# Performance work log

Hardware: AMD Instinct MI355X
Metric: run time of the kernel (lower is better)

## Reference

```python
import jax, jax.numpy as jnp
import numpy as np

K_MASK = -2.3819763e+38
NUM_KV_HEADS = 4
SOFT_CAP = 50.0
WINDOW = 1024
ROPE_BASE = 10000.0
ROPE_SCALE = 1.0


def rms_norm(x, scale=None, eps=1e-6):
    var = jnp.mean(jnp.square(x), axis=-1, keepdims=True)
    normed = x * jax.lax.rsqrt(var + eps)
    if scale is not None:
        normed = normed * (1.0 + scale)
    return normed


def apply_rope(x, positions):
    # x: [B, T, N, H], positions: [B, T]
    head_dim = x.shape[-1]
    fraction = 2.0 * jnp.arange(head_dim // 2, dtype=jnp.float32) / head_dim
    timescale = ROPE_BASE ** fraction  # [H/2]
    sinusoid = positions[..., None, None].astype(jnp.float32) / timescale / ROPE_SCALE  # [B,T,1,H/2]
    sin, cos = jnp.sin(sinusoid), jnp.cos(sinusoid)
    first, second = jnp.split(x, 2, axis=-1)
    return jnp.concatenate([first * cos - second * sin,
                            second * cos + first * sin], axis=-1).astype(x.dtype)


def setup_inputs() -> dict:
    key = jax.random.key(0)
    ks = jax.random.split(key, 8)
    B, T, D, N, K, H, F = 2, 2048, 2048, 8, NUM_KV_HEADS, 256, 8192
    CACHE = 4096
    x = jax.random.normal(ks[0], (B, T, D), dtype=jnp.float32)
    segment_pos = jnp.broadcast_to(jnp.arange(T, dtype=jnp.int32)[None, :], (B, T))
    # causal mask over cache slots: after scatter, slot s (< T) holds position s; slots >= T are empty
    s_idx = jnp.arange(CACHE)
    t_idx = jnp.arange(T)
    attn_mask = (s_idx[None, :] <= t_idx[:, None]) & (s_idx[None, :] < T)
    attn_mask = jnp.broadcast_to(attn_mask[None], (B, T, CACHE))
    cache_k = jnp.zeros((B, CACHE, K, H), dtype=jnp.float32)
    cache_v = jnp.zeros((B, CACHE, K, H), dtype=jnp.float32)
    cache_positions = jnp.zeros((B, CACHE), dtype=jnp.int32)
    end_index = jnp.zeros((B,), dtype=jnp.int32)
    w_q = jax.random.normal(ks[1], (N, D, H), dtype=jnp.float32) * 0.02
    w_kv = jax.random.normal(ks[2], (2, K, D, H), dtype=jnp.float32) * 0.02
    w_attn_vec = jax.random.normal(ks[3], (N, H, D), dtype=jnp.float32) * 0.02
    w_gating = jax.random.normal(ks[4], (2, F, D), dtype=jnp.float32) * 0.02
    w_linear = jax.random.normal(ks[5], (F, D), dtype=jnp.float32) * 0.02
    return {
        'x': x, 'segment_pos': segment_pos, 'attn_mask': attn_mask,
        'cache_k': cache_k, 'cache_v': cache_v,
        'cache_positions': cache_positions, 'end_index': end_index,
        'w_q': w_q, 'w_kv': w_kv, 'w_attn_vec': w_attn_vec,
        'q_norm_scale': jnp.zeros((H,), dtype=jnp.float32),
        'k_norm_scale': jnp.zeros((H,), dtype=jnp.float32),
        'pre_attn_scale': jnp.zeros((D,), dtype=jnp.float32),
        'post_attn_scale': jnp.zeros((D,), dtype=jnp.float32),
        'pre_ffw_scale': jnp.zeros((D,), dtype=jnp.float32),
        'post_ffw_scale': jnp.zeros((D,), dtype=jnp.float32),
        'w_gating': w_gating, 'w_linear': w_linear,
        'skip_scale': jnp.ones((1,), dtype=jnp.float32),
    }


def reference(x, segment_pos, attn_mask, cache_k, cache_v, cache_positions, end_index,
              w_q, w_kv, w_attn_vec, q_norm_scale, k_norm_scale,
              pre_attn_scale, post_attn_scale, pre_ffw_scale, post_ffw_scale,
              w_gating, w_linear, skip_scale):
    B, T, D = x.shape
    cache_size = cache_v.shape[1]

    h = rms_norm(x, pre_attn_scale)

    # --- attention ---
    q = jnp.einsum('BTD,NDH->BTNH', h, w_q)
    q = rms_norm(q, q_norm_scale)
    q = apply_rope(q, segment_pos)

    k, v = jnp.einsum('BSD,CKDH->CBSKH', h, w_kv)
    k = rms_norm(k, k_norm_scale)
    v = rms_norm(v, None)
    k = apply_rope(k, segment_pos)

    # KV-cache scatter (ring-buffer indexing)
    idx = (end_index[:, None] + jnp.arange(T)[None, :]) % cache_size  # [B,T]
    bidx = jnp.arange(B)[:, None]
    v = cache_v.at[bidx, idx].set(v)              # [B,S,K,H]
    k = cache_k.at[bidx, idx].set(k)
    cache_pos = cache_positions.at[bidx, idx].set(segment_pos)  # [B,S]

    # GQA logits
    N, H = q.shape[2], q.shape[3]
    G = N // NUM_KV_HEADS
    qg = q.reshape(B, T, NUM_KV_HEADS, G, H)
    logits = jnp.einsum('BTKGH,BSKH->BTKGS', qg, k).reshape(B, T, N, cache_size)

    # soft cap
    logits = jnp.tanh(logits / SOFT_CAP) * SOFT_CAP

    # sliding-window mask against cache positions
    sliding = (cache_pos[:, None, :] > segment_pos[:, :, None] - WINDOW) & \
              (cache_pos[:, None, :] < segment_pos[:, :, None] + WINDOW)  # [B,T,S]
    mask = attn_mask & sliding

    padded = jnp.where(mask[:, :, None, :], logits, K_MASK)
    probs = jax.nn.softmax(padded, axis=-1).astype(k.dtype)

    pg = probs.reshape(B, T, NUM_KV_HEADS, G, cache_size)
    encoded = jnp.einsum('BTKGS,BSKH->BTKGH', pg, v).reshape(B, T, N, H)
    attn_out = jnp.einsum('BTNH,NHD->BTD', encoded, w_attn_vec)

    # post-attn norm + residual (skip_scale on the skip connection)
    attn_out = rms_norm(attn_out, post_attn_scale)
    attn_out = x * skip_scale + attn_out

    # --- feed-forward ---
    ffw_in = rms_norm(attn_out, pre_ffw_scale)
    gate = jnp.einsum('BTF,CHF->BTCH', ffw_in, w_gating)  # C=2
    act = jax.nn.gelu(gate[..., 0, :]) * gate[..., 1, :]
    ffw_out = jnp.einsum('BTH,HF->BTF', act, w_linear)
    ffw_out = rms_norm(ffw_out, post_ffw_scale)

    return attn_out + ffw_out
```

## Files before the change

kernel.cpp:

```cpp
#include <hip/hip_runtime.h>


typedef _Float16 h8 __attribute__((ext_vector_type(8)));
typedef _Float16 h4 __attribute__((ext_vector_type(4)));
typedef float f4 __attribute__((ext_vector_type(4)));

#define BDIM 2
#define TDIM 2048
#define DDIM 2048
#define NQ 8
#define NKV 4
#define HDIM 256
#define FDIM 8192
#define MROWS (BDIM * TDIM)
#define WINDOW 1024

__device__ inline float gelu_tanh(float x) {
  return 0.5f * x * (1.f + tanhf(0.7978845608028654f * (x + 0.044715f * x * x * x)));
}

__device__ __forceinline__ void g2l16(const _Float16* g, _Float16* l) {
  __builtin_amdgcn_global_load_lds(
      (const __attribute__((address_space(1))) void*)g,
      (__attribute__((address_space(3))) void*)l, 16, 0, 0);
}

__device__ inline float block_sum(float v, float* sbuf) {
#pragma unroll
  for (int off = 32; off; off >>= 1) v += __shfl_xor(v, off, 64);
  __syncthreads();
  if ((threadIdx.x & 63) == 0) sbuf[threadIdx.x >> 6] = v;
  __syncthreads();
  return sbuf[0] + sbuf[1] + sbuf[2] + sbuf[3];
}

template <int EPI>
__global__ __launch_bounds__(256, 2) void gemm_bt(
    const _Float16* __restrict__ A, const _Float16* __restrict__ Bt,
    void* __restrict__ Cout, const _Float16* __restrict__ aux,
    int M, int Nc, int K) {
  __shared__ _Float16 As[128 * 32];
  __shared__ _Float16 Bs[128 * 32];
  const int tid = threadIdx.x;
  const int m0 = blockIdx.y * 128, n0 = blockIdx.x * 128;
  const int w = tid >> 6, lane = tid & 63;
  const int l16 = lane & 15, quad = lane >> 4;
  const int wm = (w >> 1) * 64, wn = (w & 1) * 64;

  f4 acc[4][4];
#pragma unroll
  for (int i = 0; i < 4; i++)
#pragma unroll
    for (int j = 0; j < 4; j++) {
      acc[i][j][0] = 0.f; acc[i][j][1] = 0.f; acc[i][j][2] = 0.f; acc[i][j][3] = 0.f;
    }

  const int lrow = lane >> 2, lcol = (lane & 3) * 8;
  const _Float16* Ag = A + (size_t)(m0 + w * 32 + lrow) * K + lcol;
  const _Float16* Bg = Bt + (size_t)(n0 + w * 32 + lrow) * K + lcol;
  _Float16* AsW = &As[(w * 32) * 32];
  _Float16* BsW = &Bs[(w * 32) * 32];

  for (int k0 = 0; k0 < K; k0 += 32) {
    __syncthreads();
    g2l16(Ag + k0,                AsW);
    g2l16(Ag + (size_t)16 * K + k0, AsW + 16 * 32);
    g2l16(Bg + k0,                BsW);
    g2l16(Bg + (size_t)16 * K + k0, BsW + 16 * 32);
    __syncthreads();
    h8 af[4], bf[4];
#pragma unroll
    for (int i = 0; i < 4; i++) af[i] = *(const h8*)&As[(wm + i * 16 + l16) * 32 + quad * 8];
#pragma unroll
    for (int i = 0; i < 4; i++) bf[i] = *(const h8*)&Bs[(wn + i * 16 + l16) * 32 + quad * 8];
#pragma unroll
    for (int mi = 0; mi < 4; mi++)
#pragma unroll
      for (int ni = 0; ni < 4; ni++)
        acc[mi][ni] = __builtin_amdgcn_mfma_f32_16x16x32_f16(af[mi], bf[ni], acc[mi][ni], 0, 0, 0);
  }

#pragma unroll
  for (int mi = 0; mi < 4; mi++)
#pragma unroll
    for (int ni = 0; ni < 4; ni++)
#pragma unroll
      for (int r = 0; r < 4; r++) {
        const int rg = m0 + wm + mi * 16 + quad * 4 + r;
        const int cg = n0 + wn + ni * 16 + l16;
        const size_t idx = (size_t)rg * Nc + cg;
        float v = acc[mi][ni][r];
        if (EPI == 0) {
          ((float*)Cout)[idx] = v;
        } else if (EPI == 1) {
          ((_Float16*)Cout)[idx] = (_Float16)v;
        } else {
          float g = (float)aux[idx];
          ((_Float16*)Cout)[idx] = (_Float16)(gelu_tanh(g) * v);
        }
      }
}

__global__ __launch_bounds__(256) void transpose_cast_kernel(
    const float* __restrict__ in, _Float16* __restrict__ out,
    int R, int C, size_t in_zstride, size_t out_zstride) {
  __shared__ float tile[64][65];
  const float* ip = in + blockIdx.z * in_zstride;
  _Float16* op = out + blockIdx.z * out_zstride;
  const int cb = blockIdx.x * 64, rb = blockIdx.y * 64;
  const int tx = threadIdx.x & 15, ty = threadIdx.x >> 4;
#pragma unroll
  for (int i = 0; i < 4; i++) {
    f4 v = *(const f4*)&ip[(size_t)(rb + ty + 16 * i) * C + cb + tx * 4];
    tile[ty + 16 * i][tx * 4 + 0] = v[0];
    tile[ty + 16 * i][tx * 4 + 1] = v[1];
    tile[ty + 16 * i][tx * 4 + 2] = v[2];
    tile[ty + 16 * i][tx * 4 + 3] = v[3];
  }
  __syncthreads();
#pragma unroll
  for (int i = 0; i < 4; i++) {
    const int c = ty + 16 * i;
    h4 o;
#pragma unroll
    for (int j = 0; j < 4; j++) o[j] = (_Float16)tile[tx * 4 + j][c];
    *(h4*)&op[(size_t)(cb + c) * R + rb + tx * 4] = o;
  }
}

__global__ void cast_fp16_kernel(const float* __restrict__ in,
                                 _Float16* __restrict__ out, int n4) {
  int i = blockIdx.x * 256 + threadIdx.x;
  if (i < n4) {
    f4 v = ((const f4*)in)[i];
    h4 o;
    o[0] = (_Float16)v[0]; o[1] = (_Float16)v[1];
    o[2] = (_Float16)v[2]; o[3] = (_Float16)v[3];
    ((h4*)out)[i] = o;
  }
}

__global__ __launch_bounds__(256) void rmsnorm_fp16_kernel(
    const float* __restrict__ in, const float* __restrict__ scale,
    _Float16* __restrict__ out) {
  __shared__ float sbuf[4];
  const int row = blockIdx.x, tid = threadIdx.x;
  const float* r = in + (size_t)row * 2048;
  f4 a = ((const f4*)r)[tid];
  f4 b = ((const f4*)r)[tid + 256];
  float ss = a[0]*a[0] + a[1]*a[1] + a[2]*a[2] + a[3]*a[3] +
             b[0]*b[0] + b[1]*b[1] + b[2]*b[2] + b[3]*b[3];
  float tot = block_sum(ss, sbuf);
  float rs = rsqrtf(tot * (1.f / 2048.f) + 1e-6f);
  f4 s0 = ((const f4*)scale)[tid];
  f4 s1 = ((const f4*)scale)[tid + 256];
  h4 o0, o1;
#pragma unroll
  for (int j = 0; j < 4; j++) {
    o0[j] = (_Float16)(a[j] * rs * (1.f + s0[j]));
    o1[j] = (_Float16)(b[j] * rs * (1.f + s1[j]));
  }
  ((h4*)(out + (size_t)row * 2048))[tid] = o0;
  ((h4*)(out + (size_t)row * 2048))[tid + 256] = o1;
}

__global__ __launch_bounds__(256) void headnorm_rope_kernel(
    const float* __restrict__ in, _Float16* __restrict__ out,
    const float* __restrict__ scale, const int* __restrict__ pos_arr,
    int heads, int do_rope, int total) {
  const int inst = blockIdx.x * 4 + (threadIdx.x >> 6);
  if (inst >= total) return;
  const int lane = threadIdx.x & 63;
  const int bt = inst / heads;
  const float* r = in + (size_t)inst * 256;
  f4 v = ((const f4*)r)[lane];
  float ss = v[0]*v[0] + v[1]*v[1] + v[2]*v[2] + v[3]*v[3];
#pragma unroll
  for (int off = 32; off; off >>= 1) ss += __shfl_xor(ss, off, 64);
  const float rs = rsqrtf(ss * (1.f / 256.f) + 1e-6f);
  f4 nv;
  if (scale) {
    f4 sc = ((const f4*)scale)[lane];
#pragma unroll
    for (int j = 0; j < 4; j++) nv[j] = v[j] * rs * (1.f + sc[j]);
  } else {
#pragma unroll
    for (int j = 0; j < 4; j++) nv[j] = v[j] * rs;
  }
  _Float16* o = out + (size_t)inst * 256;
  h4 res;
  if (do_rope) {
    const float pos = (float)pos_arr[bt];
    const bool lo = lane < 32;
#pragma unroll
    for (int j = 0; j < 4; j++) {
      float partner = __shfl_xor(nv[j], 32, 64);
      const int ph = (lane * 4 + j) & 127;
      float it = exp2f((float)ph * -0.103810253f);
      float ang = pos * it;
      float sn, cs;
      sincosf(ang, &sn, &cs);
      float val = lo ? (nv[j] * cs - partner * sn) : (nv[j] * cs + partner * sn);
      res[j] = (_Float16)val;
    }
  } else {
#pragma unroll
    for (int j = 0; j < 4; j++) res[j] = (_Float16)nv[j];
  }
  ((h4*)o)[lane] = res;
}

__global__ __launch_bounds__(256) void transpose_v_kernel(
    const _Float16* __restrict__ vbf, _Float16* __restrict__ vT) {
  __shared__ _Float16 tile[32][33];
  const int z = blockIdx.z;
  const int b = z >> 2, kvh = z & 3;
  const int tb = blockIdx.x * 32, hb = blockIdx.y * 32;
  const int x = threadIdx.x, y = threadIdx.y;
#pragma unroll
  for (int i = 0; i < 4; i++)
    tile[y + 8 * i][x] =
        vbf[(size_t)(b * TDIM + tb + y + 8 * i) * (NKV * HDIM) + kvh * HDIM + hb + x];
  __syncthreads();
#pragma unroll
  for (int i = 0; i < 4; i++)
    vT[((size_t)z * HDIM + hb + y + 8 * i) * TDIM + tb + x] = tile[x][y + 8 * i];
}

__global__ __launch_bounds__(256) void attn_kernel(
    const _Float16* __restrict__ qf, const _Float16* __restrict__ kf,
    const _Float16* __restrict__ vT, _Float16* __restrict__ enc) {
  __shared__ _Float16 Ks[32 * 256];
  __shared__ _Float16 Vs[256 * 32];
  __shared__ _Float16 Ps[4][16 * 32];
  const int t0 = blockIdx.x * 64;
  const int n = blockIdx.y;
  const int b = blockIdx.z;
  const int kvh = n >> 1;
  const int tid = threadIdx.x;
  const int w = tid >> 6, lane = tid & 63, l16 = lane & 15, quad = lane >> 4;

  h8 qfrag[8];
  {
    const int trow = t0 + w * 16 + l16;
    const _Float16* qp =
        qf + ((size_t)(b * TDIM + trow) * (NQ * HDIM)) + n * HDIM + quad * 8;
#pragma unroll
    for (int ks = 0; ks < 8; ks++) qfrag[ks] = *(const h8*)(qp + ks * 32);
  }

  f4 O[16];
#pragma unroll
  for (int i = 0; i < 16; i++) { O[i][0] = 0.f; O[i][1] = 0.f; O[i][2] = 0.f; O[i][3] = 0.f; }
  float m_i[4], l_i[4];
#pragma unroll
  for (int r = 0; r < 4; r++) { m_i[r] = -1e30f; l_i[r] = 0.f; }

  int s_begin = t0 - (WINDOW - 1);
  if (s_begin < 0) s_begin = 0;
  s_begin &= ~31;
  const int s_end = t0 + 64;
  const _Float16* kbase = kf + (size_t)b * TDIM * (NKV * HDIM) + kvh * HDIM;
  const _Float16* vbase = vT + ((size_t)(b * NKV + kvh) * HDIM) * TDIM;

  for (int s0 = s_begin; s0 < s_end; s0 += 32) {
    __syncthreads();
#pragma unroll
    for (int p = 0; p < 4; p++) {
      int g = p * 256 + tid;
      {
        int si = g >> 5, hg = (g & 31) << 3;
        *(h8*)&Ks[si * 256 + hg] = *(const h8*)(kbase + (size_t)(s0 + si) * (NKV * HDIM) + hg);
      }
      {
        int h = g >> 2, sg = (g & 3) << 3;
        *(h8*)&Vs[h * 32 + sg] = *(const h8*)(vbase + (size_t)h * TDIM + s0 + sg);
      }
    }
    __syncthreads();

    float P[2][4], cmax[4];
#pragma unroll
    for (int r = 0; r < 4; r++) cmax[r] = -1e30f;
#pragma unroll
    for (int sc = 0; sc < 2; sc++) {
      f4 lg; lg[0] = 0.f; lg[1] = 0.f; lg[2] = 0.f; lg[3] = 0.f;
#pragma unroll
      for (int ks = 0; ks < 8; ks++) {
        h8 kb = *(const h8*)&Ks[(sc * 16 + l16) * 256 + ks * 32 + quad * 8];
        lg = __builtin_amdgcn_mfma_f32_16x16x32_f16(qfrag[ks], kb, lg, 0, 0, 0);
      }
      const int scol = s0 + sc * 16 + l16;
#pragma unroll
      for (int r = 0; r < 4; r++) {
        const int trow = t0 + w * 16 + quad * 4 + r;
        float xv = 50.f * tanhf(lg[r] * 0.02f);
        bool valid = (scol <= trow) && (scol > trow - WINDOW);
        P[sc][r] = valid ? xv : -1e30f;
        cmax[r] = fmaxf(cmax[r], P[sc][r]);
      }
    }
#pragma unroll
    for (int off = 1; off < 16; off <<= 1)
#pragma unroll
      for (int r = 0; r < 4; r++) cmax[r] = fmaxf(cmax[r], __shfl_xor(cmax[r], off, 16));
    float alpha[4], psum[4];
#pragma unroll
    for (int r = 0; r < 4; r++) {
      float mnew = fmaxf(m_i[r], cmax[r]);
      alpha[r] = __expf(m_i[r] - mnew);
      m_i[r] = mnew;
      psum[r] = 0.f;
    }
#pragma unroll
    for (int sc = 0; sc < 2; sc++)
#pragma unroll
      for (int r = 0; r < 4; r++) {
        float pv = __expf(P[sc][r] - m_i[r]);
        P[sc][r] = pv;
        psum[r] += pv;
      }
#pragma unroll
    for (int off = 1; off < 16; off <<= 1)
#pragma unroll
      for (int r = 0; r < 4; r++) psum[r] += __shfl_xor(psum[r], off, 16);
#pragma unroll
    for (int r = 0; r < 4; r++) l_i[r] = l_i[r] * alpha[r] + psum[r];
#pragma unroll
    for (int i = 0; i < 16; i++)
#pragma unroll
      for (int r = 0; r < 4; r++) O[i][r] *= alpha[r];
#pragma unroll
    for (int sc = 0; sc < 2; sc++)
#pragma unroll
      for (int r = 0; r < 4; r++)
        Ps[w][(quad * 4 + r) * 32 + sc * 16 + l16] = (_Float16)P[sc][r];
    h8 pa = *(const h8*)&Ps[w][l16 * 32 + quad * 8];
#pragma unroll
    for (int ht = 0; ht < 16; ht++) {
      h8 vb = *(const h8*)&Vs[(ht * 16 + l16) * 32 + quad * 8];
      O[ht] = __builtin_amdgcn_mfma_f32_16x16x32_f16(pa, vb, O[ht], 0, 0, 0);
    }
  }

  float invl[4];
#pragma unroll
  for (int r = 0; r < 4; r++) invl[r] = 1.f / l_i[r];
#pragma unroll
  for (int ht = 0; ht < 16; ht++)
#pragma unroll
    for (int r = 0; r < 4; r++) {
      const int trow = t0 + w * 16 + quad * 4 + r;
      enc[((size_t)(b * TDIM + trow)) * (NQ * HDIM) + n * HDIM + ht * 16 + l16] =
          (_Float16)(O[ht][r] * invl[r]);
    }
}

__global__ __launch_bounds__(256) void postattn_kernel(
    const float* __restrict__ attnraw, const float* __restrict__ x,
    const float* __restrict__ post_scale, const float* __restrict__ pre_ffw_scale,
    const float* __restrict__ skip, float* __restrict__ attn_out,
    _Float16* __restrict__ ffw_in) {
  __shared__ float sbuf[4];
  const int row = blockIdx.x, tid = threadIdx.x;
  const float* ar = attnraw + (size_t)row * 2048;
  const float* xr = x + (size_t)row * 2048;
  f4 a0 = ((const f4*)ar)[tid], a1 = ((const f4*)ar)[tid + 256];
  float ss = a0[0]*a0[0] + a0[1]*a0[1] + a0[2]*a0[2] + a0[3]*a0[3] +
             a1[0]*a1[0] + a1[1]*a1[1] + a1[2]*a1[2] + a1[3]*a1[3];
  float tot = block_sum(ss, sbuf);
  float rs = rsqrtf(tot * (1.f / 2048.f) + 1e-6f);
  const float sk = skip[0];
  f4 x0 = ((const f4*)xr)[tid], x1 = ((const f4*)xr)[tid + 256];
  f4 p0 = ((const f4*)post_scale)[tid], p1 = ((const f4*)post_scale)[tid + 256];
  f4 at0, at1;
#pragma unroll
  for (int j = 0; j < 4; j++) {
    at0[j] = x0[j] * sk + a0[j] * rs * (1.f + p0[j]);
    at1[j] = x1[j] * sk + a1[j] * rs * (1.f + p1[j]);
  }
  ((f4*)(attn_out + (size_t)row * 2048))[tid] = at0;
  ((f4*)(attn_out + (size_t)row * 2048))[tid + 256] = at1;
  float ss2 = at0[0]*at0[0] + at0[1]*at0[1] + at0[2]*at0[2] + at0[3]*at0[3] +
              at1[0]*at1[0] + at1[1]*at1[1] + at1[2]*at1[2] + at1[3]*at1[3];
  float tot2 = block_sum(ss2, sbuf);
  float rs2 = rsqrtf(tot2 * (1.f / 2048.f) + 1e-6f);
  f4 f0 = ((const f4*)pre_ffw_scale)[tid], f1 = ((const f4*)pre_ffw_scale)[tid + 256];
  h4 o0, o1;
#pragma unroll
  for (int j = 0; j < 4; j++) {
    o0[j] = (_Float16)(at0[j] * rs2 * (1.f + f0[j]));
    o1[j] = (_Float16)(at1[j] * rs2 * (1.f + f1[j]));
  }
  ((h4*)(ffw_in + (size_t)row * 2048))[tid] = o0;
  ((h4*)(ffw_in + (size_t)row * 2048))[tid + 256] = o1;
}

__global__ __launch_bounds__(256) void final_kernel(
    const float* __restrict__ ffw, const float* __restrict__ attn_out,
    const float* __restrict__ post_ffw_scale, float* __restrict__ out) {
  __shared__ float sbuf[4];
  const int row = blockIdx.x, tid = threadIdx.x;
  const float* fr = ffw + (size_t)row * 2048;
  const float* ar = attn_out + (size_t)row * 2048;
  f4 a0 = ((const f4*)fr)[tid], a1 = ((const f4*)fr)[tid + 256];
  float ss = a0[0]*a0[0] + a0[1]*a0[1] + a0[2]*a0[2] + a0[3]*a0[3] +
             a1[0]*a1[0] + a1[1]*a1[1] + a1[2]*a1[2] + a1[3]*a1[3];
  float tot = block_sum(ss, sbuf);
  float rs = rsqrtf(tot * (1.f / 2048.f) + 1e-6f);
  f4 s0 = ((const f4*)post_ffw_scale)[tid], s1 = ((const f4*)post_ffw_scale)[tid + 256];
  f4 x0 = ((const f4*)ar)[tid], x1 = ((const f4*)ar)[tid + 256];
  f4 o0, o1;
#pragma unroll
  for (int j = 0; j < 4; j++) {
    o0[j] = x0[j] + a0[j] * rs * (1.f + s0[j]);
    o1[j] = x1[j] + a1[j] * rs * (1.f + s1[j]);
  }
  ((f4*)(out + (size_t)row * 2048))[tid] = o0;
  ((f4*)(out + (size_t)row * 2048))[tid + 256] = o1;
}

extern "C" void kernel_launch(void* const* d_in, const int* in_sizes, int n_in,
                              void* d_out, int out_size, void* d_ws, size_t ws_size,
                              hipStream_t stream) {
  (void)in_sizes; (void)n_in; (void)out_size; (void)ws_size;
  const float* x              = (const float*)d_in[0];
  const int*   segment_pos    = (const int*)d_in[1];
  const float* w_q            = (const float*)d_in[7];
  const float* w_kv           = (const float*)d_in[8];
  const float* w_attn_vec     = (const float*)d_in[9];
  const float* q_norm_scale   = (const float*)d_in[10];
  const float* k_norm_scale   = (const float*)d_in[11];
  const float* pre_attn_scale = (const float*)d_in[12];
  const float* post_attn_scale= (const float*)d_in[13];
  const float* pre_ffw_scale  = (const float*)d_in[14];
  const float* post_ffw_scale = (const float*)d_in[15];
  const float* w_gating       = (const float*)d_in[16];
  const float* w_linear       = (const float*)d_in[17];
  const float* skip_scale     = (const float*)d_in[18];

  char* ws = (char*)d_ws;
  const size_t MB = 1024 * 1024;
  _Float16* Wq   = (_Float16*)(ws + 0);
  _Float16* Wk   = (_Float16*)(ws + 8 * MB);
  _Float16* Wv   = (_Float16*)(ws + 12 * MB);
  _Float16* Wo   = (_Float16*)(ws + 0);
  _Float16* Wg   = (_Float16*)(ws + 0);
  _Float16* Wl   = (_Float16*)(ws + 0);
  _Float16* Hbf  = (_Float16*)(ws + 64 * MB);
  float* attnF   = (float*)(ws + 80 * MB);
  float* qf32    = (float*)(ws + 112 * MB);
  float* kf32    = (float*)(ws + 144 * MB);
  float* vf32    = (float*)(ws + 160 * MB);
  _Float16* qbf  = (_Float16*)(ws + 176 * MB);
  _Float16* kbf  = (_Float16*)(ws + 192 * MB);
  _Float16* vbf  = (_Float16*)(ws + 200 * MB);
  _Float16* enc  = (_Float16*)(ws + 208 * MB);
  float* attnraw = (float*)(ws + 224 * MB);
  _Float16* vT   = (_Float16*)(ws + 112 * MB);
  _Float16* gate0= (_Float16*)(ws + 112 * MB);
  _Float16* act  = (_Float16*)(ws + 176 * MB);
  float* ffw     = (float*)(ws + 240 * MB);
  float* outp    = (float*)d_out;

  transpose_cast_kernel<<<dim3(HDIM / 64, DDIM / 64, NQ), 256, 0, stream>>>(
      w_q, Wq, DDIM, HDIM, (size_t)DDIM * HDIM, (size_t)HDIM * DDIM);
  transpose_cast_kernel<<<dim3(HDIM / 64, DDIM / 64, NKV), 256, 0, stream>>>(
      w_kv, Wk, DDIM, HDIM, (size_t)DDIM * HDIM, (size_t)HDIM * DDIM);
  transpose_cast_kernel<<<dim3(HDIM / 64, DDIM / 64, NKV), 256, 0, stream>>>(
      w_kv + (size_t)NKV * DDIM * HDIM, Wv, DDIM, HDIM,
      (size_t)DDIM * HDIM, (size_t)HDIM * DDIM);
  rmsnorm_fp16_kernel<<<MROWS, 256, 0, stream>>>(x, pre_attn_scale, Hbf);
  gemm_bt<0><<<dim3((NQ * HDIM) / 128, MROWS / 128), 256, 0, stream>>>(
      Hbf, Wq, qf32, nullptr, MROWS, NQ * HDIM, DDIM);
  gemm_bt<0><<<dim3((NKV * HDIM) / 128, MROWS / 128), 256, 0, stream>>>(
      Hbf, Wk, kf32, nullptr, MROWS, NKV * HDIM, DDIM);
  gemm_bt<0><<<dim3((NKV * HDIM) / 128, MROWS / 128), 256, 0, stream>>>(
      Hbf, Wv, vf32, nullptr, MROWS, NKV * HDIM, DDIM);
  headnorm_rope_kernel<<<(MROWS * NQ) / 4, 256, 0, stream>>>(
      qf32, qbf, q_norm_scale, segment_pos, NQ, 1, MROWS * NQ);
  headnorm_rope_kernel<<<(MROWS * NKV) / 4, 256, 0, stream>>>(
      kf32, kbf, k_norm_scale, segment_pos, NKV, 1, MROWS * NKV);
  headnorm_rope_kernel<<<(MROWS * NKV) / 4, 256, 0, stream>>>(
      vf32, vbf, nullptr, segment_pos, NKV, 0, MROWS * NKV);
  transpose_v_kernel<<<dim3(TDIM / 32, HDIM / 32, BDIM * NKV), dim3(32, 8), 0, stream>>>(vbf, vT);
  attn_kernel<<<dim3(TDIM / 64, NQ, BDIM), 256, 0, stream>>>(qbf, kbf, vT, enc);
  transpose_cast_kernel<<<dim3(DDIM / 64, (NQ * HDIM) / 64, 1), 256, 0, stream>>>(
      w_attn_vec, Wo, NQ * HDIM, DDIM, 0, 0);
  gemm_bt<0><<<dim3(DDIM / 128, MROWS / 128), 256, 0, stream>>>(
      enc, Wo, attnraw, nullptr, MROWS, DDIM, NQ * HDIM);
  postattn_kernel<<<MROWS, 256, 0, stream>>>(attnraw, x, post_attn_scale,
                                             pre_ffw_scale, skip_scale, attnF, Hbf);
  cast_fp16_kernel<<<(2 * FDIM * DDIM / 4 + 255) / 256, 256, 0, stream>>>(
      w_gating, Wg, 2 * FDIM * DDIM / 4);
  gemm_bt<1><<<dim3(FDIM / 128, MROWS / 128), 256, 0, stream>>>(
      Hbf, Wg, gate0, nullptr, MROWS, FDIM, DDIM);
  gemm_bt<2><<<dim3(FDIM / 128, MROWS / 128), 256, 0, stream>>>(
      Hbf, Wg + (size_t)FDIM * DDIM, act, gate0, MROWS, FDIM, DDIM);
  transpose_cast_kernel<<<dim3(DDIM / 64, FDIM / 64, 1), 256, 0, stream>>>(
      w_linear, Wl, FDIM, DDIM, 0, 0);
  gemm_bt<0><<<dim3(DDIM / 128, MROWS / 128), 256, 0, stream>>>(
      act, Wl, ffw, nullptr, MROWS, DDIM, FDIM);
  final_kernel<<<MROWS, 256, 0, stream>>>(ffw, attnF, post_ffw_scale, outp);
}
```

Before: 1.337 ms.

## Fuse Q/K/V projections into one GEMM and one head-norm/RoPE kernel

```diff
diff --git a/kernel.cpp b/kernel.cpp
--- a/kernel.cpp
+++ b/kernel.cpp
@@ -14,6 +14,7 @@
 #define FDIM 8192
 #define MROWS (BDIM * TDIM)
 #define WINDOW 1024
+#define QS 4096
 
 __device__ inline float gelu_tanh(float x) {
   return 0.5f * x * (1.f + tanhf(0.7978845608028654f * (x + 0.044715f * x * x * x)));
@@ -35,7 +36,7 @@
 }
 
 template <int EPI>
-__global__ __launch_bounds__(256, 2) void gemm_bt(
+__global__ __launch_bounds__(256, 4) void gemm_bt(
     const _Float16* __restrict__ A, const _Float16* __restrict__ Bt,
     void* __restrict__ Cout, const _Float16* __restrict__ aux,
     int M, int Nc, int K) {
@@ -63,9 +64,9 @@
 
   for (int k0 = 0; k0 < K; k0 += 32) {
     __syncthreads();
-    g2l16(Ag + k0,                AsW);
+    g2l16(Ag + k0,                  AsW);
     g2l16(Ag + (size_t)16 * K + k0, AsW + 16 * 32);
-    g2l16(Bg + k0,                BsW);
+    g2l16(Bg + k0,                  BsW);
     g2l16(Bg + (size_t)16 * K + k0, BsW + 16 * 32);
     __syncthreads();
     h8 af[4], bf[4];
@@ -164,20 +165,20 @@
   ((h4*)(out + (size_t)row * 2048))[tid + 256] = o1;
 }
 
-__global__ __launch_bounds__(256) void headnorm_rope_kernel(
-    const float* __restrict__ in, _Float16* __restrict__ out,
-    const float* __restrict__ scale, const int* __restrict__ pos_arr,
-    int heads, int do_rope, int total) {
+__global__ __launch_bounds__(256) void headnorm_qkv_kernel(
+    const float* __restrict__ qkv, _Float16* __restrict__ out,
+    const float* __restrict__ qsc, const float* __restrict__ ksc,
+    const int* __restrict__ pos_arr) {
   const int inst = blockIdx.x * 4 + (threadIdx.x >> 6);
-  if (inst >= total) return;
   const int lane = threadIdx.x & 63;
-  const int bt = inst / heads;
-  const float* r = in + (size_t)inst * 256;
+  const int row = inst >> 4, slot = inst & 15;
+  const float* r = qkv + (size_t)row * QS + slot * 256;
   f4 v = ((const f4*)r)[lane];
   float ss = v[0]*v[0] + v[1]*v[1] + v[2]*v[2] + v[3]*v[3];
 #pragma unroll
   for (int off = 32; off; off >>= 1) ss += __shfl_xor(ss, off, 64);
   const float rs = rsqrtf(ss * (1.f / 256.f) + 1e-6f);
+  const float* scale = (slot < 8) ? qsc : (slot < 12 ? ksc : nullptr);
   f4 nv;
   if (scale) {
     f4 sc = ((const f4*)scale)[lane];
@@ -187,10 +188,9 @@
 #pragma unroll
     for (int j = 0; j < 4; j++) nv[j] = v[j] * rs;
   }
-  _Float16* o = out + (size_t)inst * 256;
   h4 res;
-  if (do_rope) {
-    const float pos = (float)pos_arr[bt];
+  if (slot < 12) {
+    const float pos = (float)pos_arr[row];
     const bool lo = lane < 32;
 #pragma unroll
     for (int j = 0; j < 4; j++) {
@@ -200,18 +200,18 @@
       float ang = pos * it;
       float sn, cs;
       sincosf(ang, &sn, &cs);
-      float val = lo ? (nv[j] * cs - partner * sn) : (nv[j] * cs + partner * sn);
-      res[j] = (_Float16)val;
+      res[j] = (_Float16)(lo ? (nv[j] * cs - partner * sn)
+                             : (nv[j] * cs + partner * sn));
     }
   } else {
 #pragma unroll
     for (int j = 0; j < 4; j++) res[j] = (_Float16)nv[j];
   }
-  ((h4*)o)[lane] = res;
+  ((h4*)(out + (size_t)row * QS + slot * 256))[lane] = res;
 }
 
 __global__ __launch_bounds__(256) void transpose_v_kernel(
-    const _Float16* __restrict__ vbf, _Float16* __restrict__ vT) {
+    const _Float16* __restrict__ qkvh, _Float16* __restrict__ vT) {
   __shared__ _Float16 tile[32][33];
   const int z = blockIdx.z;
   const int b = z >> 2, kvh = z & 3;
@@ -220,7 +220,7 @@
 #pragma unroll
   for (int i = 0; i < 4; i++)
     tile[y + 8 * i][x] =
-        vbf[(size_t)(b * TDIM + tb + y + 8 * i) * (NKV * HDIM) + kvh * HDIM + hb + x];
+        qkvh[(size_t)(b * TDIM + tb + y + 8 * i) * QS + 3072 + kvh * 256 + hb + x];
   __syncthreads();
 #pragma unroll
   for (int i = 0; i < 4; i++)
@@ -228,8 +228,8 @@
 }
 
 __global__ __launch_bounds__(256) void attn_kernel(
-    const _Float16* __restrict__ qf, const _Float16* __restrict__ kf,
-    const _Float16* __restrict__ vT, _Float16* __restrict__ enc) {
+    const _Float16* __restrict__ qkvh, const _Float16* __restrict__ vT,
+    _Float16* __restrict__ enc) {
   __shared__ _Float16 Ks[32 * 256];
   __shared__ _Float16 Vs[256 * 32];
   __shared__ _Float16 Ps[4][16 * 32];
@@ -244,7 +244,7 @@
   {
     const int trow = t0 + w * 16 + l16;
     const _Float16* qp =
-        qf + ((size_t)(b * TDIM + trow) * (NQ * HDIM)) + n * HDIM + quad * 8;
+        qkvh + (size_t)(b * TDIM + trow) * QS + n * HDIM + quad * 8;
 #pragma unroll
     for (int ks = 0; ks < 8; ks++) qfrag[ks] = *(const h8*)(qp + ks * 32);
   }
@@ -260,7 +260,7 @@
   if (s_begin < 0) s_begin = 0;
   s_begin &= ~31;
   const int s_end = t0 + 64;
-  const _Float16* kbase = kf + (size_t)b * TDIM * (NKV * HDIM) + kvh * HDIM;
+  const _Float16* kbase = qkvh + (size_t)b * TDIM * QS + 2048 + kvh * HDIM;
   const _Float16* vbase = vT + ((size_t)(b * NKV + kvh) * HDIM) * TDIM;
 
   for (int s0 = s_begin; s0 < s_end; s0 += 32) {
@@ -270,7 +270,7 @@
       int g = p * 256 + tid;
       {
         int si = g >> 5, hg = (g & 31) << 3;
-        *(h8*)&Ks[si * 256 + hg] = *(const h8*)(kbase + (size_t)(s0 + si) * (NKV * HDIM) + hg);
+        *(h8*)&Ks[si * 256 + hg] = *(const h8*)(kbase + (size_t)(s0 + si) * QS + hg);
       }
       {
         int h = g >> 2, sg = (g & 3) << 3;
@@ -441,50 +441,38 @@
 
   char* ws = (char*)d_ws;
   const size_t MB = 1024 * 1024;
-  _Float16* Wq   = (_Float16*)(ws + 0);
-  _Float16* Wk   = (_Float16*)(ws + 8 * MB);
-  _Float16* Wv   = (_Float16*)(ws + 12 * MB);
+  _Float16* Wqkv = (_Float16*)(ws + 0);
   _Float16* Wo   = (_Float16*)(ws + 0);
   _Float16* Wg   = (_Float16*)(ws + 0);
   _Float16* Wl   = (_Float16*)(ws + 0);
   _Float16* Hbf  = (_Float16*)(ws + 64 * MB);
   float* attnF   = (float*)(ws + 80 * MB);
-  float* qf32    = (float*)(ws + 112 * MB);
-  float* kf32    = (float*)(ws + 144 * MB);
-  float* vf32    = (float*)(ws + 160 * MB);
-  _Float16* qbf  = (_Float16*)(ws + 176 * MB);
-  _Float16* kbf  = (_Float16*)(ws + 192 * MB);
-  _Float16* vbf  = (_Float16*)(ws + 200 * MB);
+  float* qkvf32  = (float*)(ws + 112 * MB);
+  _Float16* qkvh = (_Float16*)(ws + 176 * MB);
   _Float16* enc  = (_Float16*)(ws + 208 * MB);
   float* attnraw = (float*)(ws + 224 * MB);
-  _Float16* vT   = (_Float16*)(ws + 112 * MB);
+  _Float16* vT   = (_Float16*)(ws + 240 * MB);
   _Float16* gate0= (_Float16*)(ws + 112 * MB);
   _Float16* act  = (_Float16*)(ws + 176 * MB);
   float* ffw     = (float*)(ws + 240 * MB);
   float* outp    = (float*)d_out;
 
   transpose_cast_kernel<<<dim3(HDIM / 64, DDIM / 64, NQ), 256, 0, stream>>>(
-      w_q, Wq, DDIM, HDIM, (size_t)DDIM * HDIM, (size_t)HDIM * DDIM);
+      w_q, Wqkv, DDIM, HDIM, (size_t)DDIM * HDIM, (size_t)HDIM * DDIM);
   transpose_cast_kernel<<<dim3(HDIM / 64, DDIM / 64, NKV), 256, 0, stream>>>(
-      w_kv, Wk, DDIM, HDIM, (size_t)DDIM * HDIM, (size_t)HDIM * DDIM);
+      w_kv, Wqkv + (size_t)2048 * DDIM, DDIM, HDIM,
+      (size_t)DDIM * HDIM, (size_t)HDIM * DDIM);
   transpose_cast_kernel<<<dim3(HDIM / 64, DDIM / 64, NKV), 256, 0, stream>>>(
-      w_kv + (size_t)NKV * DDIM * HDIM, Wv, DDIM, HDIM,
+      w_kv + (size_t)NKV * DDIM * HDIM, Wqkv + (size_t)3072 * DDIM, DDIM, HDIM,
       (size_t)DDIM * HDIM, (size_t)HDIM * DDIM);
   rmsnorm_fp16_kernel<<<MROWS, 256, 0, stream>>>(x, pre_attn_scale, Hbf);
-  gemm_bt<0><<<dim3((NQ * HDIM) / 128, MROWS / 128), 256, 0, stream>>>(
-      Hbf, Wq, qf32, nullptr, MROWS, NQ * HDIM, DDIM);
-  gemm_bt<0><<<dim3((NKV * HDIM) / 128, MROWS / 128), 256, 0, stream>>>(
-      Hbf, Wk, kf32, nullptr, MROWS, NKV * HDIM, DDIM);
-  gemm_bt<0><<<dim3((NKV * HDIM) / 128, MROWS / 128), 256, 0, stream>>>(
-      Hbf, Wv, vf32, nullptr, MROWS, NKV * HDIM, DDIM);
-  headnorm_rope_kernel<<<(MROWS * NQ) / 4, 256, 0, stream>>>(
-      qf32, qbf, q_norm_scale, segment_pos, NQ, 1, MROWS * NQ);
-  headnorm_rope_kernel<<<(MROWS * NKV) / 4, 256, 0, stream>>>(
-      kf32, kbf, k_norm_scale, segment_pos, NKV, 1, MROWS * NKV);
-  headnorm_rope_kernel<<<(MROWS * NKV) / 4, 256, 0, stream>>>(
-      vf32, vbf, nullptr, segment_pos, NKV, 0, MROWS * NKV);
-  transpose_v_kernel<<<dim3(TDIM / 32, HDIM / 32, BDIM * NKV), dim3(32, 8), 0, stream>>>(vbf, vT);
-  attn_kernel<<<dim3(TDIM / 64, NQ, BDIM), 256, 0, stream>>>(qbf, kbf, vT, enc);
+  gemm_bt<0><<<dim3(QS / 128, MROWS / 128), 256, 0, stream>>>(
+      Hbf, Wqkv, qkvf32, nullptr, MROWS, QS, DDIM);
+  headnorm_qkv_kernel<<<(MROWS * 16) / 4, 256, 0, stream>>>(
+      qkvf32, qkvh, q_norm_scale, k_norm_scale, segment_pos);
+  transpose_v_kernel<<<dim3(TDIM / 32, HDIM / 32, BDIM * NKV), dim3(32, 8), 0, stream>>>(
+      qkvh, vT);
+  attn_kernel<<<dim3(TDIM / 64, NQ, BDIM), 256, 0, stream>>>(qkvh, vT, enc);
   transpose_cast_kernel<<<dim3(DDIM / 64, (NQ * HDIM) / 64, 1), 256, 0, stream>>>(
       w_attn_vec, Wo, NQ * HDIM, DDIM, 0, 0);
   gemm_bt<0><<<dim3(DDIM / 128, MROWS / 128), 256, 0, stream>>>(
```

Result: faster. 1.272 ms (-4.8%).
